# Performance work log

Measured on AMD Instinct MI355X. Metric: run time of the kernel, lower is better.

Reference implementation:

```python
import jax, jax.numpy as jnp
import numpy as np

K, P, Q, D = 16, 1024, 1024, 64  # heads, value-in dim, out dim, head dim; P'=P, Q'=Q, D'=D
B, N = 2, 2048                   # batch, seq (self-attention: M=N)
TEMPERATURE = jnp.sqrt(jnp.float32(D))

def _xavier(key, shape):
    fan_in, fan_out = shape[-2], shape[-1]
    lim = jnp.sqrt(6.0 / (fan_in + fan_out))
    return jax.random.uniform(key, shape, jnp.float32, -lim, lim)

def setup_inputs() -> dict:
    key = jax.random.key(0)
    k0, k1, k2, k3, k4 = jax.random.split(key, 5)
    return {
        'y_prime': jax.random.normal(k0, (B, N, Q), jnp.float32),
        'mask': jnp.zeros((N, N), jnp.float32),  # log-domain additive mask [M,N]
        'Lam_x': _xavier(k1, (K, P, D)),  # Lambda^(x): [K,P',D']
        'Lam_y': _xavier(k2, (K, Q, D)),  # Lambda^(y): [K,Q',D']
        'Th_x': _xavier(k3, (K, P, D)),   # Theta^(x):  [K,P,D]
        'Th_y': _xavier(k4, (K, Q, D)),   # Theta^(y):  [K,Q,D]
    }

def reference(y_prime, mask, Lam_x, Lam_y, Th_x, Th_y):
    # self-attention: x' = x = y'
    x_p = y_prime
    x = x_p
    # key projection: [B,M,K,D']
    r = jnp.einsum('bmp,kpd->bmkd', x_p, Lam_x)
    # bilinear scores: [K,B,M,N]
    r = jnp.einsum('bmkd,kqd,bnq->kbmn', r, Lam_y, y_prime)
    r = r + mask[None, None, :, :]
    # softmax over M (axis=-2), scaled by sqrt(D')
    A = jax.nn.softmax(r / TEMPERATURE, axis=-2)
    # value aggregation: [B,N,K,D]
    r = jnp.einsum('kbmn,bmp,kpd->bnkd', A, x, Th_x)
    # output projection: [B,N,Q]
    return jnp.einsum('bnkd,kqd->bnq', r, Th_y)
```

## Files before the change

### kernel.cpp

```cpp
#include <hip/hip_runtime.h>
#include <hip/hip_bf16.h>

#define KH 16
#define PD 1024
#define QD 1024
#define DD 64
#define BB 2
#define NN 2048
#define BN 4096
#define ST 72
#define SOFT_C 12.0f
#define LOG2E 1.4426950408889634f
#define SOFT_C2 17.312340490667560f

typedef unsigned short u16;
typedef __attribute__((ext_vector_type(8))) short bf16x8;
typedef __attribute__((ext_vector_type(4))) short bf16x4;
typedef __attribute__((ext_vector_type(4))) float f32x4;

__device__ __forceinline__ float bf2f(u16 u) {
    return __uint_as_float(((unsigned)u) << 16);
}
__device__ __forceinline__ u16 f2bf(float f) {
    unsigned x = __float_as_uint(f);
    x += 0x7FFFu + ((x >> 16) & 1u);
    return (u16)(x >> 16);
}
__device__ __forceinline__ f32x4 mfma_k32(bf16x8 a, bf16x8 b, f32x4 c) {
    return __builtin_amdgcn_mfma_f32_16x16x32_bf16(a, b, c, 0, 0, 0);
}
__device__ __forceinline__ bf16x8 ldfrag(const u16* base, int r0, int kc, int lane) {
    return *reinterpret_cast<const bf16x8*>(base + (r0 + (lane & 15)) * ST + kc +
                                            ((lane >> 4) << 3));
}
__device__ __forceinline__ bf16x8 ldfragL(const u16* base, int r0, int kc, int lane) {
    return *reinterpret_cast<const bf16x8*>(base + ((r0 + (lane & 15)) << 6) + kc +
                                            ((lane >> 4) << 3));
}
__device__ __forceinline__ bf16x4 pack4(float a, float b, float c, float d) {
    union { bf16x4 v; __hip_bfloat162 h[2]; } u;
    u.h[0] = __float22bfloat162_rn(make_float2(a, b));
    u.h[1] = __float22bfloat162_rn(make_float2(c, d));
    return u.v;
}
__device__ __forceinline__ void gl_lds16(const u16* g, u16* l) {
    __builtin_amdgcn_global_load_lds(
        (const __attribute__((address_space(1))) void*)g,
        (__attribute__((address_space(3))) void*)l, 16, 0, 0);
}
template <int ROWS>
__device__ __forceinline__ void stage_dma(const u16* __restrict__ src, int ld,
                                          u16* dst, int lane, int w) {
#pragma unroll
    for (int c = 0; c < ROWS / 32; ++c) {
        int rbase = (w * (ROWS / 32) + c) * 8;
        const u16* g = src + (size_t)(rbase + (lane >> 3)) * ld + ((lane & 7) << 3);
        gl_lds16(g, dst + (rbase << 6));
    }
}

__global__ void detect_kernel(const u16* __restrict__ y, int* flag, int* mnz) {
    __shared__ int cnt;
    if (threadIdx.x == 0) cnt = 0;
    __syncthreads();
    int local = 0;
    for (int i = threadIdx.x; i < 8192; i += 256) {
        u16 u = y[i];
        int e = (u >> 7) & 0xFF;
        if (u == 0 || (e >= 96 && e < 160)) local++;
    }
    atomicAdd(&cnt, local);
    __syncthreads();
    if (threadIdx.x == 0) {
        *flag = (cnt > 7372) ? 1 : 0;
        *mnz = 0;
    }
}

__global__ __launch_bounds__(256) void prep_kernel(
    const void* __restrict__ ysrc, const void* __restrict__ msrc,
    const void* __restrict__ s0, const void* __restrict__ s1,
    const void* __restrict__ s2, const void* __restrict__ s3,
    u16* __restrict__ ycan, u16* __restrict__ LamXt, u16* __restrict__ LamYt,
    u16* __restrict__ ThXt, u16* __restrict__ ThYr, u16* __restrict__ maskc,
    const int* __restrict__ flag, int* __restrict__ mnz) {
    int z = blockIdx.z, bx = blockIdx.x, tid = threadIdx.x;
    int isbf = *flag;
    if (z == 0) {
        size_t n4 = (size_t)NN * NN / 8;
        if (!isbf) n4 *= 2;
        const uint4* p = (const uint4*)msrc;
        unsigned acc = 0;
        for (size_t i = (size_t)bx * 256 + tid; i < n4; i += 256 * 256) {
            uint4 v = p[i];
            acc |= v.x | v.y | v.z | v.w;
        }
        if (acc) atomicOr(mnz, 1);
    } else if (z == 1) {
        int n = BN * PD;
        for (int i = (bx * 256 + tid) * 4; i < n; i += 256 * 256 * 4) {
            if (isbf) {
                *reinterpret_cast<uint2*>(ycan + i) =
                    *reinterpret_cast<const uint2*>((const u16*)ysrc + i);
            } else {
                float4 f = *reinterpret_cast<const float4*>((const float*)ysrc + i);
                u16 t[4] = {f2bf(f.x), f2bf(f.y), f2bf(f.z), f2bf(f.w)};
                *reinterpret_cast<uint2*>(ycan + i) = *reinterpret_cast<uint2*>(t);
            }
        }
    } else if (z <= 4) {
        const void* src = (z == 2) ? s0 : (z == 3) ? s1 : s2;
        u16* dst = (z == 2) ? LamXt : (z == 3) ? LamYt : ThXt;
        float scale = (z == 3) ? 0.125f : 1.0f;
        int k = bx >> 4, p0 = (bx & 15) * 64;
        __shared__ float T[64][65];
        const u16* s16 = (const u16*)src + ((size_t)k * PD + p0) * DD;
        const float* s32 = (const float*)src + ((size_t)k * PD + p0) * DD;
#pragma unroll
        for (int it = 0; it < 2; ++it) {
            int chunk = it * 256 + tid;
            int row = chunk >> 3, c8 = (chunk & 7) << 3;
            float f[8];
            if (isbf) {
                uint4 v = *reinterpret_cast<const uint4*>(s16 + row * DD + c8);
                u16 t[8];
                *reinterpret_cast<uint4*>(t) = v;
#pragma unroll
                for (int e = 0; e < 8; ++e) f[e] = bf2f(t[e]);
            } else {
                float4 a = *reinterpret_cast<const float4*>(s32 + row * DD + c8);
                float4 b = *reinterpret_cast<const float4*>(s32 + row * DD + c8 + 4);
                f[0] = a.x; f[1] = a.y; f[2] = a.z; f[3] = a.w;
                f[4] = b.x; f[5] = b.y; f[6] = b.z; f[7] = b.w;
            }
#pragma unroll
            for (int e = 0; e < 8; ++e) T[row][c8 + e] = f[e] * scale;
        }
        __syncthreads();
        u16* drow = dst + (size_t)k * DD * PD + p0;
#pragma unroll
        for (int it = 0; it < 2; ++it) {
            int chunk = it * 256 + tid;
            int d = chunk >> 3, c8 = (chunk & 7) << 3;
            u16 t[8];
#pragma unroll
            for (int e = 0; e < 8; ++e) t[e] = f2bf(T[c8 + e][d]);
            *reinterpret_cast<uint4*>(drow + (size_t)d * PD + c8) =
                *reinterpret_cast<uint4*>(t);
        }
    } else if (z == 5) {
        int k = bx >> 4, q0 = (bx & 15) * 64;
#pragma unroll
        for (int it = 0; it < 2; ++it) {
            int chunk = it * 256 + tid;
            int row = chunk >> 3, c8 = (chunk & 7) << 3;
            size_t si = ((size_t)k * QD + q0 + row) * DD + c8;
            u16 t[8];
            if (isbf) {
                *reinterpret_cast<uint4*>(t) =
                    *reinterpret_cast<const uint4*>((const u16*)s3 + si);
            } else {
                float4 a = *reinterpret_cast<const float4*>((const float*)s3 + si);
                float4 b = *reinterpret_cast<const float4*>((const float*)s3 + si + 4);
                t[0] = f2bf(a.x); t[1] = f2bf(a.y); t[2] = f2bf(a.z); t[3] = f2bf(a.w);
                t[4] = f2bf(b.x); t[5] = f2bf(b.y); t[6] = f2bf(b.z); t[7] = f2bf(b.w);
            }
            *reinterpret_cast<uint4*>(ThYr + (size_t)(q0 + row) * (KH * DD) +
                                      k * DD + c8) = *reinterpret_cast<uint4*>(t);
        }
    } else {
        size_t n8 = (size_t)NN * NN / 8;
        for (size_t c = (size_t)bx * 256 + tid; c < n8; c += 256 * 256) {
            size_t i = c * 8;
            float f[8];
            if (isbf) {
                uint4 v = *reinterpret_cast<const uint4*>((const u16*)msrc + i);
                u16 t[8];
                *reinterpret_cast<uint4*>(t) = v;
#pragma unroll
                for (int e = 0; e < 8; ++e) f[e] = bf2f(t[e]);
            } else {
                float4 a = *reinterpret_cast<const float4*>((const float*)msrc + i);
                float4 b = *reinterpret_cast<const float4*>((const float*)msrc + i + 4);
                f[0] = a.x; f[1] = a.y; f[2] = a.z; f[3] = a.w;
                f[4] = b.x; f[5] = b.y; f[6] = b.z; f[7] = b.w;
            }
            u16 t[8];
#pragma unroll
            for (int e = 0; e < 8; ++e) t[e] = f2bf(f[e] * 0.125f);
            *reinterpret_cast<uint4*>(maskc + i) = *reinterpret_cast<uint4*>(t);
        }
    }
}

__global__ __launch_bounds__(256, 3) void proj_gemm(
    const u16* __restrict__ A,
    const u16* __restrict__ Bm,
    u16* __restrict__ Xk, u16* __restrict__ Yk, u16* __restrict__ Vtg) {
    int tid = threadIdx.x, lane = tid & 63, w = tid >> 6;
    int mhalf = w & 1, nhalf = w >> 1;
    int m0 = blockIdx.x * 128, n0 = blockIdx.y * 128;
    __shared__ u16 As[128 * 64];
    __shared__ u16 Bs[128 * 64];
    f32x4 acc[4][4] = {};

    for (int kk = 0; kk < PD; kk += 64) {
        __syncthreads();
        stage_dma<128>(A + (size_t)m0 * PD + kk, PD, As, lane, w);
        stage_dma<128>(Bm + (size_t)n0 * PD + kk, PD, Bs, lane, w);
        __syncthreads();
#pragma unroll
        for (int kc = 0; kc < 64; kc += 32) {
            bf16x8 af[4], bf[4];
#pragma unroll
            for (int i = 0; i < 4; ++i) af[i] = ldfragL(As, mhalf * 64 + i * 16, kc, lane);
#pragma unroll
            for (int j = 0; j < 4; ++j) bf[j] = ldfragL(Bs, nhalf * 64 + j * 16, kc, lane);
#pragma unroll
            for (int i = 0; i < 4; ++i)
#pragma unroll
                for (int j = 0; j < 4; ++j) acc[i][j] = mfma_k32(af[i], bf[j], acc[i][j]);
        }
    }
    int s = n0 >> 10;
    int quad = lane >> 4, col = lane & 15;
    u16* stg = nhalf ? Bs : As;
    __syncthreads();
    if (s == 2) {
#pragma unroll
        for (int i = 0; i < 4; ++i)
#pragma unroll
            for (int j = 0; j < 4; ++j)
                *reinterpret_cast<bf16x4*>(stg + ((mhalf * 2 + (i >> 1)) * 4 + j) * 512 +
                                           quad * 128 + col * 8 + (i & 1) * 4) =
                    pack4(acc[i][j][0], acc[i][j][1], acc[i][j][2], acc[i][j][3]);
    } else {
#pragma unroll
        for (int i = 0; i < 4; ++i)
#pragma unroll
            for (int j = 0; j < 4; ++j)
#pragma unroll
                for (int reg = 0; reg < 4; ++reg)
                    stg[(mhalf * 64 + i * 16 + quad * 4 + reg) * 64 + j * 16 + col] =
                        f2bf(acc[i][j][reg]);
    }
    __syncthreads();
#pragma unroll
    for (int h = 0; h < 2; ++h) {
        int kh = ((n0 + h * 64) >> 6) & 15;
        const u16* src = h ? Bs : As;
        if (s == 2) {
            u16* vb = Vtg + (size_t)kh * DD * BN + (size_t)m0 * 64;
#pragma unroll
            for (int it = 0; it < 4; ++it) {
                int chunk = it * 256 + tid;
                *reinterpret_cast<uint4*>(vb + chunk * 8) =
                    *reinterpret_cast<const uint4*>(src + chunk * 8);
            }
        } else {
            u16* ob = (s == 0 ? Xk : Yk) + (size_t)kh * BN * DD + (size_t)m0 * DD;
#pragma unroll
            for (int it = 0; it < 4; ++it) {
                int chunk = it * 256 + tid;
                *reinterpret_cast<uint4*>(ob + chunk * 8) =
                    *reinterpret_cast<const uint4*>(src + chunk * 8);
            }
        }
    }
}

__global__ __launch_bounds__(512, 4) void attn_kernel(
    const u16* __restrict__ Xk,
    const u16* __restrict__ Yk,
    const u16* __restrict__ Vtg,
    const u16* __restrict__ maskc,
    const int* __restrict__ mnz,
    u16* __restrict__ O) {
    int tid = threadIdx.x, lane = tid & 63, w = tid >> 6;
    int quad = lane >> 4, col = lane & 15;
    int H = blockIdx.x;
    int L = (H & 7) * 64 + (H >> 3);
    int q0 = (L & 15) * 128, k = (L >> 4) & 15, b = L >> 8;
    const u16* Qp = Yk + ((size_t)k * BN + b * NN + q0) * DD;
    const u16* Kp = Xk + ((size_t)k * BN + b * NN) * DD;
    const u16* Vh = Vtg + (size_t)k * DD * BN + (size_t)b * NN * 64;
    __shared__ u16 Kb[3][64 * ST];
    __shared__ u16 Ost[128 * ST];
    int mz = *mnz;

    const u16* qrow = Qp + (size_t)(w * 16 + col) * DD + (quad << 3);
    bf16x8 qf0 = *reinterpret_cast<const bf16x8*>(qrow);
    bf16x8 qf1 = *reinterpret_cast<const bf16x8*>(qrow + 32);

    int srow = tid >> 3, scol = (tid & 7) << 3;
    const u16* kgp = Kp + (size_t)srow * DD + scol;
    int soff = srow * ST + scol;

    uint4 kr = *reinterpret_cast<const uint4*>(kgp);
    *reinterpret_cast<uint4*>(Kb[0] + soff) = kr;
    kr = *reinterpret_cast<const uint4*>(kgp + (size_t)64 * DD);
    __syncthreads();

    float lp = 0.0f;
    f32x4 oacc[4] = {};

    for (int t = 0; t < 32; ++t) {
        int cur = t % 3;
        if (t < 31) {
            int nxt = (t + 1) % 3;
            *reinterpret_cast<uint4*>(Kb[nxt] + soff) = kr;
            __syncthreads();
        }
        const u16* Ks = Kb[cur];
        const u16* vt = Vh + t * 4096;
        bf16x8 av[2][4];
#pragma unroll
        for (int half = 0; half < 2; ++half)
#pragma unroll
            for (int dg = 0; dg < 4; ++dg)
                av[half][dg] = *reinterpret_cast<const bf16x8*>(
                    vt + half * 2048 + dg * 512 + lane * 8);
        if (t < 30) kr = *reinterpret_cast<const uint4*>(kgp + (size_t)(t + 2) * 64 * DD);
        int m0 = t * 64;

        bf16x4 pb4[4];
#pragma unroll
        for (int kg = 0; kg < 4; ++kg) {
            bf16x8 a0 = ldfrag(Ks, kg * 16, 0, lane);
            bf16x8 a1 = ldfrag(Ks, kg * 16, 32, lane);
            f32x4 s = {};
            s = mfma_k32(a0, qf0, s);
            s = mfma_k32(a1, qf1, s);
            if (mz) {
#pragma unroll
                for (int reg = 0; reg < 4; ++reg)
                    s[reg] += bf2f(
                        maskc[(size_t)(m0 + kg * 16 + quad * 4 + reg) * NN + q0 +
                              w * 16 + col]);
            }
            float p0 = exp2f(fmaf(s[0], LOG2E, -SOFT_C2));
            float p1 = exp2f(fmaf(s[1], LOG2E, -SOFT_C2));
            float p2 = exp2f(fmaf(s[2], LOG2E, -SOFT_C2));
            float p3 = exp2f(fmaf(s[3], LOG2E, -SOFT_C2));
            lp += (p0 + p1) + (p2 + p3);
            pb4[kg] = pack4(p0, p1, p2, p3);
        }
#pragma unroll
        for (int half = 0; half < 2; ++half) {
            bf16x8 pb8 = __builtin_shufflevector(pb4[half * 2], pb4[half * 2 + 1],
                                                 0, 1, 2, 3, 4, 5, 6, 7);
#pragma unroll
            for (int dg = 0; dg < 4; ++dg)
                oacc[dg] = mfma_k32(av[half][dg], pb8, oacc[dg]);
        }
    }

    float l = lp;
    l += __shfl_xor(l, 16);
    l += __shfl_xor(l, 32);
    float inv = 1.0f / l;
    int q = w * 16 + col;
#pragma unroll
    for (int dg = 0; dg < 4; ++dg)
        *reinterpret_cast<bf16x4*>(Ost + q * ST + dg * 16 + quad * 4) =
            pack4(oacc[dg][0] * inv, oacc[dg][1] * inv, oacc[dg][2] * inv,
                  oacc[dg][3] * inv);
    __syncthreads();
#pragma unroll
    for (int it = 0; it < 2; ++it) {
        int chunk = it * 512 + tid;
        int row = chunk >> 3, c8 = (chunk & 7) << 3;
        *reinterpret_cast<uint4*>(O + (size_t)(b * NN + q0 + row) * (KH * DD) +
                                  k * DD + c8) =
            *reinterpret_cast<const uint4*>(Ost + row * ST + c8);
    }
}

__global__ __launch_bounds__(256, 3) void out_gemm(
    const u16* __restrict__ A,
    const u16* __restrict__ Bm,
    const int* __restrict__ flag,
    void* __restrict__ outv) {
    int tid = threadIdx.x, lane = tid & 63, w = tid >> 6;
    int mhalf = w & 1, nhalf = w >> 1;
    int m0 = blockIdx.x * 128, n0 = blockIdx.y * 128;
    __shared__ u16 S[2][128 * 64];
    u16* As = S[0];
    u16* Bs = S[1];
    f32x4 acc[4][4] = {};

    for (int kk = 0; kk < KH * DD; kk += 64) {
        __syncthreads();
        stage_dma<128>(A + (size_t)m0 * (KH * DD) + kk, KH * DD, As, lane, w);
        stage_dma<128>(Bm + (size_t)n0 * (KH * DD) + kk, KH * DD, Bs, lane, w);
        __syncthreads();
#pragma unroll
        for (int kc = 0; kc < 64; kc += 32) {
            bf16x8 af[4], bf[4];
#pragma unroll
            for (int i = 0; i < 4; ++i) af[i] = ldfragL(As, mhalf * 64 + i * 16, kc, lane);
#pragma unroll
            for (int j = 0; j < 4; ++j) bf[j] = ldfragL(Bs, nhalf * 64 + j * 16, kc, lane);
#pragma unroll
            for (int i = 0; i < 4; ++i)
#pragma unroll
                for (int j = 0; j < 4; ++j) acc[i][j] = mfma_k32(af[i], bf[j], acc[i][j]);
        }
    }
    int isbf = *flag;
    int quad = lane >> 4, col = lane & 15;
    if (isbf) {
#pragma unroll
        for (int i = 0; i < 4; ++i)
#pragma unroll
            for (int j = 0; j < 4; ++j)
#pragma unroll
                for (int reg = 0; reg < 4; ++reg) {
                    size_t row = m0 + mhalf * 64 + i * 16 + quad * 4 + reg;
                    int c = n0 + nhalf * 64 + j * 16 + col;
                    ((u16*)outv)[row * QD + c] = f2bf(acc[i][j][reg]);
                }
    } else {
        float* Sf = (float*)&S[0][0];
#pragma unroll
        for (int h = 0; h < 2; ++h) {
            __syncthreads();
            if (mhalf == h) {
#pragma unroll
                for (int i = 0; i < 4; ++i)
#pragma unroll
                    for (int j = 0; j < 4; ++j)
#pragma unroll
                        for (int reg = 0; reg < 4; ++reg)
                            Sf[(i * 16 + quad * 4 + reg) * 128 + nhalf * 64 +
                               j * 16 + col] = acc[i][j][reg];
            }
            __syncthreads();
            float* orow = (float*)outv + (size_t)(m0 + h * 64) * QD + n0;
#pragma unroll
            for (int it = 0; it < 8; ++it) {
                int chunk = it * 256 + tid;
                int row = chunk >> 5, c4 = (chunk & 31) * 4;
                *reinterpret_cast<float4*>(orow + (size_t)row * QD + c4) =
                    *reinterpret_cast<const float4*>(Sf + row * 128 + c4);
            }
        }
    }
}

extern "C" void kernel_launch(void* const* d_in, const int* in_sizes, int n_in,
                              void* d_out, int out_size, void* d_ws, size_t ws_size,
                              hipStream_t stream) {
    char* wsb = (char*)d_ws;
    int* flag = (int*)wsb;
    int* mnz = (int*)(wsb + 16);
    u16* ycan = (u16*)(wsb + 64);
    const size_t NYP = (size_t)BN * PD;
    const size_t NW = (size_t)KH * PD * DD;
    const size_t OSZ = (size_t)BN * KH * DD;
    u16* Wcat = ycan + NYP;
    u16* ThYr = Wcat + 3 * NW;
    u16* Xk = ThYr + NW;
    u16* Yk = Xk + OSZ;
    u16* Vtg = Yk + OSZ;
    u16* maskc = Vtg + OSZ;
    u16* Ob = ycan;

    detect_kernel<<<1, 256, 0, stream>>>((const u16*)d_in[0], flag, mnz);
    prep_kernel<<<dim3(256, 1, 7), 256, 0, stream>>>(
        d_in[0], d_in[1], d_in[2], d_in[3], d_in[4], d_in[5], ycan, Wcat,
        Wcat + NW, Wcat + 2 * NW, ThYr, maskc, flag, mnz);
    proj_gemm<<<dim3(BN / 128, 3072 / 128), 256, 0, stream>>>(ycan, Wcat, Xk, Yk, Vtg);
    attn_kernel<<<512, 512, 0, stream>>>(Xk, Yk, Vtg, maskc, mnz, Ob);
    out_gemm<<<dim3(BN / 128, QD / 128), 256, 0, stream>>>(Ob, ThYr, flag, d_out);
}
```

Measured before the change: 234.2 us.

## Double attention query tile per block and skip mask conversion when mask is zero

The attention kernel now gives each wave 32 query columns instead of 16. Each block therefore covers 256 queries, and the grid shrinks to 256 blocks, so every K tile and V fragment loaded is reused across two query groups. The mask zero-scan moves into its own kernel that runs before prep, which lets prep skip converting the mask to bf16 when it is all zero. The change also adds s_setprio around the PV MFMA phase. The costs are higher register pressure (launch bounds lowered to 2), fewer blocks to fill the GPU, and one extra kernel launch.

```diff
diff --git a/kernel.cpp b/kernel.cpp
--- a/kernel.cpp
+++ b/kernel.cpp
@@ -77,26 +77,30 @@
     }
 }
 
+__global__ __launch_bounds__(256) void scan_kernel(const void* __restrict__ msrc,
+                                                   const int* __restrict__ flag,
+                                                   int* __restrict__ mnz) {
+    size_t n4 = (size_t)NN * NN / 8;
+    if (!*flag) n4 *= 2;
+    const uint4* p = (const uint4*)msrc;
+    unsigned acc = 0;
+    for (size_t i = (size_t)blockIdx.x * 256 + threadIdx.x; i < n4; i += 256 * 256) {
+        uint4 v = p[i];
+        acc |= v.x | v.y | v.z | v.w;
+    }
+    if (acc) atomicOr(mnz, 1);
+}
+
 __global__ __launch_bounds__(256) void prep_kernel(
     const void* __restrict__ ysrc, const void* __restrict__ msrc,
     const void* __restrict__ s0, const void* __restrict__ s1,
     const void* __restrict__ s2, const void* __restrict__ s3,
     u16* __restrict__ ycan, u16* __restrict__ LamXt, u16* __restrict__ LamYt,
     u16* __restrict__ ThXt, u16* __restrict__ ThYr, u16* __restrict__ maskc,
-    const int* __restrict__ flag, int* __restrict__ mnz) {
+    const int* __restrict__ flag, const int* __restrict__ mnz) {
     int z = blockIdx.z, bx = blockIdx.x, tid = threadIdx.x;
     int isbf = *flag;
     if (z == 0) {
-        size_t n4 = (size_t)NN * NN / 8;
-        if (!isbf) n4 *= 2;
-        const uint4* p = (const uint4*)msrc;
-        unsigned acc = 0;
-        for (size_t i = (size_t)bx * 256 + tid; i < n4; i += 256 * 256) {
-            uint4 v = p[i];
-            acc |= v.x | v.y | v.z | v.w;
-        }
-        if (acc) atomicOr(mnz, 1);
-    } else if (z == 1) {
         int n = BN * PD;
         for (int i = (bx * 256 + tid) * 4; i < n; i += 256 * 256 * 4) {
             if (isbf) {
@@ -108,10 +112,10 @@
                 *reinterpret_cast<uint2*>(ycan + i) = *reinterpret_cast<uint2*>(t);
             }
         }
-    } else if (z <= 4) {
-        const void* src = (z == 2) ? s0 : (z == 3) ? s1 : s2;
-        u16* dst = (z == 2) ? LamXt : (z == 3) ? LamYt : ThXt;
-        float scale = (z == 3) ? 0.125f : 1.0f;
+    } else if (z <= 3) {
+        const void* src = (z == 1) ? s0 : (z == 2) ? s1 : s2;
+        u16* dst = (z == 1) ? LamXt : (z == 2) ? LamYt : ThXt;
+        float scale = (z == 2) ? 0.125f : 1.0f;
         int k = bx >> 4, p0 = (bx & 15) * 64;
         __shared__ float T[64][65];
         const u16* s16 = (const u16*)src + ((size_t)k * PD + p0) * DD;
@@ -148,7 +152,7 @@
             *reinterpret_cast<uint4*>(drow + (size_t)d * PD + c8) =
                 *reinterpret_cast<uint4*>(t);
         }
-    } else if (z == 5) {
+    } else if (z == 4) {
         int k = bx >> 4, q0 = (bx & 15) * 64;
 #pragma unroll
         for (int it = 0; it < 2; ++it) {
@@ -169,6 +173,7 @@
                                       k * DD + c8) = *reinterpret_cast<uint4*>(t);
         }
     } else {
+        if (*mnz == 0) return;
         size_t n8 = (size_t)NN * NN / 8;
         for (size_t c = (size_t)bx * 256 + tid; c < n8; c += 256 * 256) {
             size_t i = c * 8;
@@ -269,7 +274,7 @@
     }
 }
 
-__global__ __launch_bounds__(512, 4) void attn_kernel(
+__global__ __launch_bounds__(512, 2) void attn_kernel(
     const u16* __restrict__ Xk,
     const u16* __restrict__ Yk,
     const u16* __restrict__ Vtg,
@@ -279,18 +284,22 @@
     int tid = threadIdx.x, lane = tid & 63, w = tid >> 6;
     int quad = lane >> 4, col = lane & 15;
     int H = blockIdx.x;
-    int L = (H & 7) * 64 + (H >> 3);
-    int q0 = (L & 15) * 128, k = (L >> 4) & 15, b = L >> 8;
+    int L = (H & 7) * 32 + (H >> 3);
+    int q0 = (L & 7) * 256, k = (L >> 3) & 15, b = L >> 7;
     const u16* Qp = Yk + ((size_t)k * BN + b * NN + q0) * DD;
     const u16* Kp = Xk + ((size_t)k * BN + b * NN) * DD;
     const u16* Vh = Vtg + (size_t)k * DD * BN + (size_t)b * NN * 64;
     __shared__ u16 Kb[3][64 * ST];
-    __shared__ u16 Ost[128 * ST];
+    __shared__ u16 Ost[256 * ST];
     int mz = *mnz;
 
-    const u16* qrow = Qp + (size_t)(w * 16 + col) * DD + (quad << 3);
-    bf16x8 qf0 = *reinterpret_cast<const bf16x8*>(qrow);
-    bf16x8 qf1 = *reinterpret_cast<const bf16x8*>(qrow + 32);
+    bf16x8 qf[2][2];
+#pragma unroll
+    for (int qg = 0; qg < 2; ++qg) {
+        const u16* qrow = Qp + (size_t)(w * 32 + qg * 16 + col) * DD + (quad << 3);
+        qf[qg][0] = *reinterpret_cast<const bf16x8*>(qrow);
+        qf[qg][1] = *reinterpret_cast<const bf16x8*>(qrow + 32);
+    }
 
     int srow = tid >> 3, scol = (tid & 7) << 3;
     const u16* kgp = Kp + (size_t)srow * DD + scol;
@@ -301,8 +310,8 @@
     kr = *reinterpret_cast<const uint4*>(kgp + (size_t)64 * DD);
     __syncthreads();
 
-    float lp = 0.0f;
-    f32x4 oacc[4] = {};
+    float lp[2] = {0.0f, 0.0f};
+    f32x4 oacc[4][2] = {};
 
     for (int t = 0; t < 32; ++t) {
         int cur = t % 3;
@@ -315,59 +324,74 @@
         const u16* vt = Vh + t * 4096;
         bf16x8 av[2][4];
 #pragma unroll
-        for (int half = 0; half < 2; ++half)
+        for (int hlf = 0; hlf < 2; ++hlf)
 #pragma unroll
             for (int dg = 0; dg < 4; ++dg)
-                av[half][dg] = *reinterpret_cast<const bf16x8*>(
-                    vt + half * 2048 + dg * 512 + lane * 8);
-        if (t < 30) kr = *reinterpret_cast<const uint4*>(kgp + (size_t)(t + 2) * 64 * DD);
+                av[hlf][dg] = *reinterpret_cast<const bf16x8*>(
+                    vt + hlf * 2048 + dg * 512 + lane * 8);
+        if (t < 30)
+            kr = *reinterpret_cast<const uint4*>(kgp + (size_t)(t + 2) * 64 * DD);
         int m0 = t * 64;
 
-        bf16x4 pb4[4];
+        bf16x4 pb4[4][2];
 #pragma unroll
         for (int kg = 0; kg < 4; ++kg) {
             bf16x8 a0 = ldfrag(Ks, kg * 16, 0, lane);
             bf16x8 a1 = ldfrag(Ks, kg * 16, 32, lane);
-            f32x4 s = {};
-            s = mfma_k32(a0, qf0, s);
-            s = mfma_k32(a1, qf1, s);
-            if (mz) {
-#pragma unroll
-                for (int reg = 0; reg < 4; ++reg)
-                    s[reg] += bf2f(
-                        maskc[(size_t)(m0 + kg * 16 + quad * 4 + reg) * NN + q0 +
-                              w * 16 + col]);
-            }
-            float p0 = exp2f(fmaf(s[0], LOG2E, -SOFT_C2));
-            float p1 = exp2f(fmaf(s[1], LOG2E, -SOFT_C2));
-            float p2 = exp2f(fmaf(s[2], LOG2E, -SOFT_C2));
-            float p3 = exp2f(fmaf(s[3], LOG2E, -SOFT_C2));
-            lp += (p0 + p1) + (p2 + p3);
-            pb4[kg] = pack4(p0, p1, p2, p3);
-        }
-#pragma unroll
-        for (int half = 0; half < 2; ++half) {
-            bf16x8 pb8 = __builtin_shufflevector(pb4[half * 2], pb4[half * 2 + 1],
-                                                 0, 1, 2, 3, 4, 5, 6, 7);
+#pragma unroll
+            for (int qg = 0; qg < 2; ++qg) {
+                f32x4 s = {};
+                s = mfma_k32(a0, qf[qg][0], s);
+                s = mfma_k32(a1, qf[qg][1], s);
+                if (mz) {
+#pragma unroll
+                    for (int reg = 0; reg < 4; ++reg)
+                        s[reg] += bf2f(
+                            maskc[(size_t)(m0 + kg * 16 + quad * 4 + reg) * NN +
+                                  q0 + w * 32 + qg * 16 + col]);
+                }
+                float p0 = exp2f(fmaf(s[0], LOG2E, -SOFT_C2));
+                float p1 = exp2f(fmaf(s[1], LOG2E, -SOFT_C2));
+                float p2 = exp2f(fmaf(s[2], LOG2E, -SOFT_C2));
+                float p3 = exp2f(fmaf(s[3], LOG2E, -SOFT_C2));
+                lp[qg] += (p0 + p1) + (p2 + p3);
+                pb4[kg][qg] = pack4(p0, p1, p2, p3);
+            }
+        }
+        __builtin_amdgcn_s_setprio(1);
+#pragma unroll
+        for (int hlf = 0; hlf < 2; ++hlf) {
+            bf16x8 pb8[2];
+#pragma unroll
+            for (int qg = 0; qg < 2; ++qg)
+                pb8[qg] = __builtin_shufflevector(pb4[hlf * 2][qg],
+                                                  pb4[hlf * 2 + 1][qg],
+                                                  0, 1, 2, 3, 4, 5, 6, 7);
 #pragma unroll
             for (int dg = 0; dg < 4; ++dg)
-                oacc[dg] = mfma_k32(av[half][dg], pb8, oacc[dg]);
-        }
-    }
-
-    float l = lp;
-    l += __shfl_xor(l, 16);
-    l += __shfl_xor(l, 32);
-    float inv = 1.0f / l;
-    int q = w * 16 + col;
-#pragma unroll
-    for (int dg = 0; dg < 4; ++dg)
-        *reinterpret_cast<bf16x4*>(Ost + q * ST + dg * 16 + quad * 4) =
-            pack4(oacc[dg][0] * inv, oacc[dg][1] * inv, oacc[dg][2] * inv,
-                  oacc[dg][3] * inv);
+#pragma unroll
+                for (int qg = 0; qg < 2; ++qg)
+                    oacc[dg][qg] = mfma_k32(av[hlf][dg], pb8[qg], oacc[dg][qg]);
+        }
+        __builtin_amdgcn_s_setprio(0);
+    }
+
+#pragma unroll
+    for (int qg = 0; qg < 2; ++qg) {
+        float l = lp[qg];
+        l += __shfl_xor(l, 16);
+        l += __shfl_xor(l, 32);
+        float inv = 1.0f / l;
+        int q = w * 32 + qg * 16 + col;
+#pragma unroll
+        for (int dg = 0; dg < 4; ++dg)
+            *reinterpret_cast<bf16x4*>(Ost + q * ST + dg * 16 + quad * 4) =
+                pack4(oacc[dg][qg][0] * inv, oacc[dg][qg][1] * inv,
+                      oacc[dg][qg][2] * inv, oacc[dg][qg][3] * inv);
+    }
     __syncthreads();
 #pragma unroll
-    for (int it = 0; it < 2; ++it) {
+    for (int it = 0; it < 4; ++it) {
         int chunk = it * 512 + tid;
         int row = chunk >> 3, c8 = (chunk & 7) << 3;
         *reinterpret_cast<uint4*>(O + (size_t)(b * NN + q0 + row) * (KH * DD) +
@@ -467,10 +491,11 @@
     u16* Ob = ycan;
 
     detect_kernel<<<1, 256, 0, stream>>>((const u16*)d_in[0], flag, mnz);
-    prep_kernel<<<dim3(256, 1, 7), 256, 0, stream>>>(
+    scan_kernel<<<256, 256, 0, stream>>>(d_in[1], flag, mnz);
+    prep_kernel<<<dim3(256, 1, 6), 256, 0, stream>>>(
         d_in[0], d_in[1], d_in[2], d_in[3], d_in[4], d_in[5], ycan, Wcat,
         Wcat + NW, Wcat + 2 * NW, ThYr, maskc, flag, mnz);
     proj_gemm<<<dim3(BN / 128, 3072 / 128), 256, 0, stream>>>(ycan, Wcat, Xk, Yk, Vtg);
-    attn_kernel<<<512, 512, 0, stream>>>(Xk, Yk, Vtg, maskc, mnz, Ob);
+    attn_kernel<<<256, 512, 0, stream>>>(Xk, Yk, Vtg, maskc, mnz, Ob);
     out_gemm<<<dim3(BN / 128, QD / 128), 256, 0, stream>>>(Ob, ThYr, flag, d_out);
 }
```

Result: no change. 238.1 us (+1.7%).
